# Performance work log

Measured on AMD Instinct MI355X. Metric: run time of the kernel, lower is better.

The kernel has to match this reference:

```python
import jax, jax.numpy as jnp
import numpy as np
from jax import lax

EPS = 1e-5

def _ln(x, w, b):
    m = jnp.mean(x, axis=-1, keepdims=True)
    v = jnp.mean((x - m) ** 2, axis=-1, keepdims=True)
    return (x - m) / jnp.sqrt(v + EPS) * w + b

def setup_inputs() -> dict:
    key = jax.random.key(0)
    ks = jax.random.split(key, 16)
    B, H, W, C = 4, 128, 128, 96
    N = H * W
    hidden = 192          # int(2.0 * dim)
    qk = 48               # dim // 2
    x = jax.random.normal(ks[0], (B, N, C), dtype=jnp.float32)
    # LayerNorm params
    norm_w = jnp.ones((C,), jnp.float32); norm_b = jnp.zeros((C,), jnp.float32)
    n1_w = jnp.ones((C,), jnp.float32); n1_b = jnp.zeros((C,), jnp.float32)
    n2_w = jnp.ones((C,), jnp.float32); n2_b = jnp.zeros((C,), jnp.float32)
    # Linear weights stored as [in, out]
    Wh = jax.random.normal(ks[1], (C, hidden), jnp.float32) * 0.02
    bh = jnp.zeros((hidden,), jnp.float32)
    Wqk = jax.random.normal(ks[2], (C, qk), jnp.float32) * 0.02
    bqk = jnp.zeros((qk,), jnp.float32)
    proj_w = jax.random.normal(ks[3], (C, C), jnp.float32) * 0.02
    proj_b = jnp.zeros((C,), jnp.float32)
    # per-branch affine on qk (init: normal std 0.02 / zeros, as in torch code)
    g1 = jax.random.normal(ks[4], (2, qk), jnp.float32) * 0.02
    be1 = jnp.zeros((2, qk), jnp.float32)
    g2 = jax.random.normal(ks[5], (2, qk), jnp.float32) * 0.02
    be2 = jnp.zeros((2, qk), jnp.float32)
    # SR convs (OIHW), kaiming-like init fan_out = k*k*C
    sr1_w = jax.random.normal(ks[6], (C, C, 8, 8), jnp.float32) * np.sqrt(2.0 / (8 * 8 * C))
    sr1_b = jnp.zeros((C,), jnp.float32)
    sr2_w = jax.random.normal(ks[7], (C, C, 4, 4), jnp.float32) * np.sqrt(2.0 / (4 * 4 * C))
    sr2_b = jnp.zeros((C,), jnp.float32)
    return dict(x=x, H=H, W=W, norm_w=norm_w, norm_b=norm_b, Wh=Wh, bh=bh,
                Wqk=Wqk, bqk=bqk, g1=g1, be1=be1, g2=g2, be2=be2,
                sr1_w=sr1_w, sr1_b=sr1_b, sr2_w=sr2_w, sr2_b=sr2_b,
                n1_w=n1_w, n1_b=n1_b, n2_w=n2_w, n2_b=n2_b,
                proj_w=proj_w, proj_b=proj_b)

def _sr_branch(xmap, cw, cb, lw, lb, stride):
    # xmap: [B,C,H,W]; strided conv with kernel==stride, then LN+GELU over tokens
    y = lax.conv_general_dilated(xmap, cw, (stride, stride), 'VALID',
                                 dimension_numbers=('NCHW', 'OIHW', 'NCHW'))
    y = y + cb[:, None, None]
    B, C = y.shape[0], y.shape[1]
    y = y.reshape(B, C, -1).transpose(0, 2, 1)  # [B, N', C]
    return jax.nn.gelu(_ln(y, lw, lb), approximate=False)

def reference(x, H, W, norm_w, norm_b, Wh, bh, Wqk, bqk, g1, be1, g2, be2,
              sr1_w, sr1_b, sr2_w, sr2_b, n1_w, n1_b, n2_w, n2_b, proj_w, proj_b):
    B, N, C = x.shape
    half = C // 2  # C // num_heads with num_heads=2
    nx = _ln(x, norm_w, norm_b)
    h = jax.nn.silu(nx @ Wh + bh)              # [B,N,2C]
    v, gate = h[..., :C], h[..., C:]
    xmap = nx.transpose(0, 2, 1).reshape(B, C, H, W)
    x1 = _sr_branch(xmap, sr1_w, sr1_b, n1_w, n1_b, 8)   # [B, N/64, C]
    x2 = _sr_branch(xmap, sr2_w, sr2_b, n2_w, n2_b, 4)   # [B, N/16, C]
    Z1 = jax.nn.silu(x1 @ Wqk + bqk)           # [B,N1,qk]
    QK1 = Z1[..., None, :] * g1 + be1          # [B,N1,2,qk]
    q1, k1 = QK1[..., 0, :], QK1[..., 1, :]
    Z2 = jax.nn.silu(x2 @ Wqk + bqk)
    QK2 = Z2[..., None, :] * g2 + be2
    q2, k2 = QK2[..., 0, :], QK2[..., 1, :]
    inv_n = 1.0 / N
    a1 = jnp.einsum('bnd,bmd->bnm', v[..., :half], q1) * inv_n
    A1 = jnp.square(jax.nn.relu(a1))
    V1 = jnp.einsum('bnm,bmd->bnd', A1, k1)
    a2 = jnp.einsum('bnd,bmd->bnm', v[..., half:], q2) * inv_n
    A2 = jnp.square(jax.nn.relu(a2))
    V2 = jnp.einsum('bnm,bmd->bnd', A2, k2)
    xc = jnp.concatenate([V1, V2], axis=-1)    # [B,N,C]
    value = xc * gate
    out = value @ proj_w + proj_b
    return out + xc
```

## Files before the change

### kernel.cpp

```cpp
#include <hip/hip_runtime.h>
#include <math.h>

#define NB   4
#define IH   128
#define IW   128
#define NTOK 16384
#define CC   96
#define HID  192
#define QKD  48
#define EPSF 1e-5f
#define INV_N (1.0f/16384.0f)

typedef __attribute__((ext_vector_type(8))) short sh8;
typedef __attribute__((ext_vector_type(4))) short ush4;
typedef __attribute__((ext_vector_type(4))) float f32x4;

__device__ __forceinline__ float wave_sum64(float v){
    #pragma unroll
    for (int off = 32; off > 0; off >>= 1) v += __shfl_xor(v, off, 64);
    return v;
}
__device__ __forceinline__ float siluf(float x){ return x / (1.0f + __expf(-x)); }
__device__ __forceinline__ float geluf(float x){ return 0.5f*x*(1.0f + erff(x*0.7071067811865475f)); }

__device__ __forceinline__ unsigned short f2bf(float f){
    union { float f; unsigned u; } x; x.f = f;
    unsigned u = x.u + 0x7FFFu + ((x.u >> 16) & 1u);
    return (unsigned short)(u >> 16);
}
__device__ __forceinline__ float b2f(unsigned hi16){
    union { unsigned u; float f; } c; c.u = hi16; return c.f;
}
__device__ __forceinline__ unsigned cvtpk(float a, float b){
    unsigned r;
    asm("v_cvt_pk_bf16_f32 %0, %1, %2" : "=v"(r) : "v"(a), "v"(b));
    return r;
}
__device__ __forceinline__ void swap32(unsigned &x, unsigned &y){
    asm volatile("v_permlane32_swap_b32 %0, %1" : "+v"(x), "+v"(y));
}
__device__ __forceinline__ void swap16(unsigned &x, unsigned &y){
    asm volatile("v_permlane16_swap_b32 %0, %1" : "+v"(x), "+v"(y));
}

__global__ __launch_bounds__(256) void k_ln(const float* __restrict__ x,
                                            const float* __restrict__ w,
                                            const float* __restrict__ bb,
                                            unsigned short* __restrict__ nxbf,
                                            unsigned short* __restrict__ nxim,
                                            const float* __restrict__ s1, unsigned short* __restrict__ d1, int n1,
                                            const float* __restrict__ s2, unsigned short* __restrict__ d2, int n2){
    int bid = blockIdx.x;
    if (bid >= 16384){
        int i4 = ((bid - 16384)*256 + threadIdx.x)*4;
        if (i4 < n1){
            float4 v = *(const float4*)(s1 + i4);
            unsigned u0 = cvtpk(v.x, v.y), u1 = cvtpk(v.z, v.w);
            ush4 o = {(short)u0, (short)(u0>>16), (short)u1, (short)(u1>>16)};
            *(ush4*)(d1 + i4) = o;
        } else {
            int j = i4 - n1;
            if (j < n2){
                float4 v = *(const float4*)(s2 + j);
                unsigned u0 = cvtpk(v.x, v.y), u1 = cvtpk(v.z, v.w);
                ush4 o = {(short)u0, (short)(u0>>16), (short)u1, (short)(u1>>16)};
                *(ush4*)(d2 + j) = o;
            }
        }
        return;
    }
    __shared__ unsigned short tile[4][96];
    int r = threadIdx.x >> 6;
    int row = bid*4 + r;
    int l = threadIdx.x & 63;
    const float* xr = x + (size_t)row*CC;
    float a = xr[l];
    float b = (l < 32) ? xr[64+l] : 0.0f;
    float s = wave_sum64(a + b);
    float m = s * (1.0f/96.0f);
    float d1f = a - m;
    float d2f = b - m;
    float sq = d1f*d1f + ((l < 32) ? d2f*d2f : 0.0f);
    float var = wave_sum64(sq) * (1.0f/96.0f);
    float rstd = rsqrtf(var + EPSF);
    unsigned short b1 = f2bf(d1f*rstd*w[l] + bb[l]);
    nxbf[(size_t)row*CC + l] = b1;
    tile[r][l] = b1;
    if (l < 32){
        unsigned short b2 = f2bf(d2f*rstd*w[64+l] + bb[64+l]);
        nxbf[(size_t)row*CC + 64 + l] = b2;
        tile[r][64+l] = b2;
    }
    __syncthreads();
    int t = threadIdx.x;
    if (t < 96){
        int row0 = bid*4;
        int bb2 = row0 >> 14, hw = row0 & 16383;
        ush4 v = {(short)tile[0][t], (short)tile[1][t], (short)tile[2][t], (short)tile[3][t]};
        *(ush4*)(nxim + (((size_t)(bb2*96 + t)) << 14) + hw) = v;
    }
}

__device__ __forceinline__ void conv_body(const unsigned short* __restrict__ nxim,
                                          const unsigned short* __restrict__ wbf,
                                          float* __restrict__ part,
                                          int posLog, int pdimLog, int pszLog,
                                          int kTotal, int rb, int split,
                                          unsigned short* pt, unsigned short* wt){
    const int NCH = 6;
    int tid = threadIdx.x;
    int lane = tid & 63, wid = tid >> 6, lo = lane & 15, g = lane >> 4;
    int psz = 1 << pszLog, pdim = 1 << pdimLog;
    int ksLog = 2*pszLog;
    int kb0 = split * 384;
    int cinc = (64 >> ksLog) << 14;

    int j   = tid & 15;
    int coff = (j*4) >> ksLog;
    int s   = (j*4) & (psz*psz - 1);
    int sy  = s >> pszLog, sx = s & (psz-1);
    int pAddr[4], pOff[4];
    #pragma unroll
    for (int i = 0; i < 4; i++){
        int p = (tid >> 4) + 16*i;
        int R = rb*64 + p;
        int b = R >> posLog, pp = R & ((1 << posLog) - 1);
        int pi = pp >> pdimLog, pj = pp & (pdim-1);
        pAddr[i] = (((b*96 + coff) + (kb0 >> ksLog)) << 14) + (pi*psz + sy)*IW + pj*psz + sx;
        pOff[i]  = p*72 + j*4;
    }
    int jj = tid & 7;
    int wAddr[3], wOff[3];
    #pragma unroll
    for (int i = 0; i < 3; i++){
        int o = (tid >> 3) + 32*i;
        wAddr[i] = o*kTotal + kb0 + jj*8;
        wOff[i]  = o*72 + jj*8;
    }

    f32x4 acc[6];
    #pragma unroll
    for (int ct = 0; ct < 6; ct++) acc[ct] = (f32x4){0.f,0.f,0.f,0.f};

    ush4 pr[4]; sh8 wr[3];
    #pragma unroll
    for (int i = 0; i < 4; i++) pr[i] = *(const ush4*)(nxim + pAddr[i]);
    #pragma unroll
    for (int i = 0; i < 3; i++) wr[i] = *(const sh8*)(wbf + wAddr[i]);

    for (int ch = 0; ch < NCH; ch++){
        __syncthreads();
        #pragma unroll
        for (int i = 0; i < 4; i++) *(ush4*)&pt[pOff[i]] = pr[i];
        #pragma unroll
        for (int i = 0; i < 3; i++) *(sh8*)&wt[wOff[i]] = wr[i];
        if (ch < NCH-1){
            #pragma unroll
            for (int i = 0; i < 4; i++){ pAddr[i] += cinc; pr[i] = *(const ush4*)(nxim + pAddr[i]); }
            #pragma unroll
            for (int i = 0; i < 3; i++){ wAddr[i] += 64;  wr[i] = *(const sh8*)(wbf + wAddr[i]); }
        }
        __syncthreads();

        sh8 a0 = *(const sh8*)&pt[(wid*16 + lo)*72 + g*8];
        sh8 a1 = *(const sh8*)&pt[(wid*16 + lo)*72 + 32 + g*8];
        #pragma unroll
        for (int ct = 0; ct < 6; ct++){
            sh8 b0 = *(const sh8*)&wt[(ct*16 + lo)*72 + g*8];
            sh8 b1 = *(const sh8*)&wt[(ct*16 + lo)*72 + 32 + g*8];
            acc[ct] = __builtin_amdgcn_mfma_f32_16x16x32_bf16(a0, b0, acc[ct], 0, 0, 0);
            acc[ct] = __builtin_amdgcn_mfma_f32_16x16x32_bf16(a1, b1, acc[ct], 0, 0, 0);
        }
    }

    int rowsTotal = NB << posLog;
    #pragma unroll
    for (int ct = 0; ct < 6; ct++){
        int o = ct*16 + lo;
        #pragma unroll
        for (int jx = 0; jx < 4; jx++){
            int R = rb*64 + wid*16 + g*4 + jx;
            part[((size_t)split*rowsTotal + R)*96 + o] = acc[ct][jx];
        }
    }
}

__global__ __launch_bounds__(256) void k_mid(const unsigned short* __restrict__ nxbf,
                                             const unsigned short* __restrict__ nxim,
                                             const float* __restrict__ Wh,
                                             const float* __restrict__ bh,
                                             const unsigned short* __restrict__ w1bf,
                                             const unsigned short* __restrict__ w2bf,
                                             unsigned short* __restrict__ vbuf,
                                             unsigned short* __restrict__ gate,
                                             float* __restrict__ part1,
                                             float* __restrict__ part2){
    __shared__ unsigned short smem[192*100];
    int bid = blockIdx.x;
    if (bid < 512){
        unsigned short* pt = smem;
        unsigned short* wt = smem + 64*72;
        if (bid < 256) conv_body(nxim, w1bf, part1, 8, 4, 3, 6144, bid & 15, bid >> 4, pt, wt);
        else { int b2 = bid - 256; conv_body(nxim, w2bf, part2, 10, 5, 2, 1536, b2 & 63, b2 >> 6, pt, wt); }
        return;
    }
    unsigned short* whbf = smem;
    int tid  = threadIdx.x;
    int lane = tid & 63;
    int wid  = tid >> 6;
    int lo   = lane & 15;
    int g    = lane >> 4;
    int row0 = (bid - 512)*64 + wid*16;

    #pragma unroll
    for (int it = 0; it < 36; it++){
        int pidx = tid + it*256;
        int k = pidx / 96, cp = (pidx - k*96)*2;
        float2 v = *(const float2*)&Wh[k*HID + cp];
        unsigned u = cvtpk(v.x, v.y);
        whbf[cp*100 + k]     = (unsigned short)u;
        whbf[(cp+1)*100 + k] = (unsigned short)(u >> 16);
    }

    sh8 a[3];
    {
        const unsigned short* ar = nxbf + (size_t)(row0 + lo)*CC;
        #pragma unroll
        for (int kc = 0; kc < 3; kc++)
            a[kc] = *(const sh8*)(ar + kc*32 + g*8);
    }
    __syncthreads();

    f32x4 acc[12];
    #pragma unroll
    for (int ct = 0; ct < 12; ct++) acc[ct] = (f32x4){0.f,0.f,0.f,0.f};
    #pragma unroll
    for (int ct = 0; ct < 12; ct++){
        #pragma unroll
        for (int kc = 0; kc < 3; kc++){
            sh8 bw = *(const sh8*)&whbf[(ct*16 + lo)*100 + kc*32 + g*8];
            acc[ct] = __builtin_amdgcn_mfma_f32_16x16x32_bf16(a[kc], bw, acc[ct], 0, 0, 0);
        }
    }

    #pragma unroll
    for (int ct = 0; ct < 12; ct++){
        int col = ct*16 + lo;
        float bcol = bh[col];
        #pragma unroll
        for (int j = 0; j < 4; j++){
            size_t row = row0 + g*4 + j;
            float hv = siluf(acc[ct][j] + bcol);
            unsigned short hb = (unsigned short)cvtpk(hv, hv);
            if (col < 96) vbuf[row*CC + col] = hb;
            else          gate[row*CC + col - 96] = hb;
        }
    }
}

__global__ __launch_bounds__(64) void k_reduce(const float* __restrict__ part1,
                                               const float* __restrict__ part2,
                                               const float* __restrict__ cb1, const float* __restrict__ cb2,
                                               const float* __restrict__ lw1, const float* __restrict__ lw2,
                                               const float* __restrict__ lb1, const float* __restrict__ lb2,
                                               const float* __restrict__ wqk,
                                               const float* __restrict__ bqk,
                                               const float* __restrict__ g1, const float* __restrict__ g2,
                                               const float* __restrict__ be1, const float* __restrict__ be2,
                                               unsigned short* __restrict__ qp1, unsigned short* __restrict__ qp2,
                                               unsigned short* __restrict__ kt1, unsigned short* __restrict__ kt2){
    __shared__ float xsh[96];
    int bid = blockIdx.x;
    bool fst = bid < 1024;
    int row   = fst ? bid : bid - 1024;
    int nsplit= fst ? 16 : 4;
    int rows  = fst ? 1024 : 4096;
    int Mper  = fst ? 256 : 1024;
    const float* part = fst ? part1 : part2;
    const float* cbias= fst ? cb1 : cb2;
    const float* lw   = fst ? lw1 : lw2;
    const float* lb   = fst ? lb1 : lb2;
    const float* g    = fst ? g1 : g2;
    const float* be   = fst ? be1 : be2;
    unsigned short* qp = fst ? qp1 : qp2;
    unsigned short* ktp= fst ? kt1 : kt2;

    int l = threadIdx.x;
    float y1 = 0.0f, y2 = 0.0f;
    for (int s = 0; s < nsplit; s++){
        const float* pr = part + ((size_t)s*rows + row)*96;
        y1 += pr[l];
        if (l < 32) y2 += pr[64+l];
    }
    y1 += cbias[l];
    if (l < 32) y2 += cbias[64+l];
    float s = wave_sum64(y1 + ((l < 32) ? y2 : 0.0f));
    float m = s * (1.0f/96.0f);
    float d1 = y1 - m, d2 = y2 - m;
    float var = wave_sum64(d1*d1 + ((l < 32) ? d2*d2 : 0.0f)) * (1.0f/96.0f);
    float rstd = rsqrtf(var + EPSF);
    xsh[l] = geluf(d1*rstd*lw[l] + lb[l]);
    if (l < 32) xsh[64+l] = geluf(d2*rstd*lw[64+l] + lb[64+l]);
    __syncthreads();
    if (l < 48){
        float z = bqk[l];
        #pragma unroll 4
        for (int c = 0; c < 96; c++) z += xsh[c]*wqk[c*48 + l];
        z = siluf(z);
        float qv = (z*g[l]    + be[l]) * INV_N;
        float kv =  z*g[48+l] + be[48+l];
        int b = row / Mper, p = row - b*Mper;
        qp[(size_t)row*64 + l] = f2bf(qv);
        ktp[((size_t)b*48 + l)*Mper + p] = f2bf(kv);
    } else {
        qp[(size_t)row*64 + l] = 0;
    }
}

__global__ __launch_bounds__(256) void k_attn(const unsigned short* __restrict__ vbuf,
                                              const unsigned short* __restrict__ qp1,
                                              const unsigned short* __restrict__ ktp1,
                                              const unsigned short* __restrict__ qp2,
                                              const unsigned short* __restrict__ ktp2,
                                              unsigned short* __restrict__ V1,
                                              unsigned short* __restrict__ V2){
    __shared__ unsigned short qs[2][64*72];
    __shared__ unsigned short ks[2][48*72];

    int bx   = blockIdx.x;
    int kind = (bx < 512) ? 1 : 0;
    int blk  = (bx < 512) ? bx : bx - 512;
    int tid  = threadIdx.x;
    int wid  = tid >> 6;
    int lane = tid & 63;
    int lo   = lane & 15;
    int g    = lane >> 4;
    int row0 = blk*128 + wid*32;
    int b    = row0 >> 14;

    int   M    = kind ? 1024 : 256;
    const unsigned short* qp = (kind ? qp2 : qp1) + (size_t)b*M*64;
    const unsigned short* kt = (kind ? ktp2 : ktp1) + (size_t)b*48*M;
    int   voff = kind ? 48 : 0;
    unsigned short* vout = kind ? V2 : V1;

    sh8 vb[2][2];
    #pragma unroll
    for (int nt = 0; nt < 2; nt++){
        const unsigned short* vrow = vbuf + (size_t)(row0 + nt*16 + lo)*CC + voff;
        vb[nt][0] = *(const sh8*)(vrow + g*8);
        if (g < 2) vb[nt][1] = *(const sh8*)(vrow + 32 + g*8);
        else { sh8 z = {0,0,0,0,0,0,0,0}; vb[nt][1] = z; }
    }

    int qm_ = tid >> 3, qc_ = tid & 7;
    int kd_ = tid >> 3, km_ = tid & 7;
    bool k2 = tid < 128;

    f32x4 acc[2][3];
    #pragma unroll
    for (int nt = 0; nt < 2; nt++)
        #pragma unroll
        for (int dt = 0; dt < 3; dt++) acc[nt][dt] = (f32x4){0.f,0.f,0.f,0.f};

    int nchunk = M >> 6;
    sh8 qr0 = *(const sh8*)(qp + (size_t)qm_*64 + qc_*8);
    sh8 qr1 = *(const sh8*)(qp + (size_t)(32 + qm_)*64 + qc_*8);
    sh8 kr0 = *(const sh8*)(kt + (size_t)kd_*M + km_*8);
    sh8 kr1;
    if (k2) kr1 = *(const sh8*)(kt + (size_t)(32 + kd_)*M + km_*8);

    for (int ch = 0; ch < nchunk; ch++){
        int bs = ch & 1;
        unsigned short* qb = qs[bs];
        unsigned short* kb = ks[bs];
        *(sh8*)&qb[qm_*72 + qc_*8] = qr0;
        *(sh8*)&qb[(32 + qm_)*72 + qc_*8] = qr1;
        *(sh8*)&kb[kd_*72 + km_*8] = kr0;
        if (k2) *(sh8*)&kb[(32 + kd_)*72 + km_*8] = kr1;
        __syncthreads();
        if (ch + 1 < nchunk){
            int mb2 = (ch + 1)*64;
            qr0 = *(const sh8*)(qp + (size_t)(mb2 + qm_)*64 + qc_*8);
            qr1 = *(const sh8*)(qp + (size_t)(mb2 + 32 + qm_)*64 + qc_*8);
            kr0 = *(const sh8*)(kt + (size_t)kd_*M + mb2 + km_*8);
            if (k2) kr1 = *(const sh8*)(kt + (size_t)(32 + kd_)*M + mb2 + km_*8);
        }

        f32x4 c[4][2];
        #pragma unroll
        for (int mt = 0; mt < 4; mt++){
            sh8 aq0 = *(const sh8*)&qb[(mt*16 + lo)*72 + g*8];
            sh8 aq1 = *(const sh8*)&qb[(mt*16 + lo)*72 + 32 + g*8];
            #pragma unroll
            for (int nt = 0; nt < 2; nt++){
                f32x4 cc = (f32x4){0.f,0.f,0.f,0.f};
                cc = __builtin_amdgcn_mfma_f32_16x16x32_bf16(aq0, vb[nt][0], cc, 0,0,0);
                cc = __builtin_amdgcn_mfma_f32_16x16x32_bf16(aq1, vb[nt][1], cc, 0,0,0);
                c[mt][nt] = cc;
            }
        }

        sh8 pa0[2], pa1[2];
        #pragma unroll
        for (int nt = 0; nt < 2; nt++){
            #pragma unroll
            for (int h = 0; h < 2; h++){
                f32x4 cm0 = c[h*2][nt];
                f32x4 cm1 = c[h*2+1][nt];
                float p00 = fmaxf(cm0[0], 0.f); p00 *= p00;
                float p01 = fmaxf(cm0[1], 0.f); p01 *= p01;
                float p02 = fmaxf(cm0[2], 0.f); p02 *= p02;
                float p03 = fmaxf(cm0[3], 0.f); p03 *= p03;
                float p10 = fmaxf(cm1[0], 0.f); p10 *= p10;
                float p11 = fmaxf(cm1[1], 0.f); p11 *= p11;
                float p12 = fmaxf(cm1[2], 0.f); p12 *= p12;
                float p13 = fmaxf(cm1[3], 0.f); p13 *= p13;
                unsigned a0 = cvtpk(p00, p01);
                unsigned a1 = cvtpk(p02, p03);
                unsigned b0 = cvtpk(p10, p11);
                unsigned b1 = cvtpk(p12, p13);
                swap32(a0, b0); swap16(a0, b0);
                swap32(a1, b1); swap16(a1, b1);
                union { unsigned u[4]; sh8 v; } pk;
                pk.u[0] = a0; pk.u[1] = a1; pk.u[2] = b0; pk.u[3] = b1;
                if (h == 0) pa0[nt] = pk.v; else pa1[nt] = pk.v;
            }
        }

        #pragma unroll
        for (int dt = 0; dt < 3; dt++){
            sh8 bk0 = *(const sh8*)&kb[(dt*16 + lo)*72 + g*8];
            sh8 bk1 = *(const sh8*)&kb[(dt*16 + lo)*72 + 32 + g*8];
            #pragma unroll
            for (int nt = 0; nt < 2; nt++){
                acc[nt][dt] = __builtin_amdgcn_mfma_f32_16x16x32_bf16(pa0[nt], bk0, acc[nt][dt], 0, 0, 0);
                acc[nt][dt] = __builtin_amdgcn_mfma_f32_16x16x32_bf16(pa1[nt], bk1, acc[nt][dt], 0, 0, 0);
            }
        }
    }

    #pragma unroll
    for (int nt = 0; nt < 2; nt++)
        #pragma unroll
        for (int dt = 0; dt < 3; dt++)
            #pragma unroll
            for (int j = 0; j < 4; j++)
                vout[(size_t)(row0 + nt*16 + g*4 + j)*48 + dt*16 + lo] =
                    (unsigned short)cvtpk(acc[nt][dt][j], acc[nt][dt][j]);
}

__global__ __launch_bounds__(256) void k_final(const unsigned short* __restrict__ V1,
                                               const unsigned short* __restrict__ V2,
                                               const unsigned short* __restrict__ gate,
                                               const float* __restrict__ projw,
                                               const float* __restrict__ projb,
                                               float* __restrict__ out){
    __shared__ unsigned short pjbf[96*100];
    int tid  = threadIdx.x;
    int lane = tid & 63;
    int wid  = tid >> 6;
    int lo   = lane & 15;
    int g    = lane >> 4;
    int row0 = blockIdx.x*64 + wid*16;

    #pragma unroll
    for (int it = 0; it < 18; it++){
        int pidx = tid + it*256;
        int k = pidx / 48, cp = (pidx - k*48)*2;
        float2 v = *(const float2*)&projw[k*CC + cp];
        unsigned u = cvtpk(v.x, v.y);
        pjbf[cp*100 + k]     = (unsigned short)u;
        pjbf[(cp+1)*100 + k] = (unsigned short)(u >> 16);
    }

    sh8 a[3];
    {
        size_t row = row0 + lo;
        const unsigned short* gr = gate + row*CC;
        #pragma unroll
        for (int kc = 0; kc < 3; kc++){
            int d0 = kc*32 + g*8;
            const unsigned short* xsrc = (d0 < 48) ? (V1 + row*48 + d0) : (V2 + row*48 + d0 - 48);
            union { sh8 v; unsigned u[4]; } xu, gu, pk;
            xu.v = *(const sh8*)xsrc;
            gu.v = *(const sh8*)(gr + d0);
            #pragma unroll
            for (int i = 0; i < 4; i++){
                float xl = b2f(xu.u[i] << 16),        xh = b2f(xu.u[i] & 0xffff0000u);
                float gl = b2f(gu.u[i] << 16),        gh = b2f(gu.u[i] & 0xffff0000u);
                pk.u[i] = cvtpk(xl*gl, xh*gh);
            }
            a[kc] = pk.v;
        }
    }
    __syncthreads();

    f32x4 acc[6];
    #pragma unroll
    for (int ct = 0; ct < 6; ct++) acc[ct] = (f32x4){0.f,0.f,0.f,0.f};
    #pragma unroll
    for (int ct = 0; ct < 6; ct++){
        #pragma unroll
        for (int kc = 0; kc < 3; kc++){
            sh8 bw = *(const sh8*)&pjbf[(ct*16 + lo)*100 + kc*32 + g*8];
            acc[ct] = __builtin_amdgcn_mfma_f32_16x16x32_bf16(a[kc], bw, acc[ct], 0, 0, 0);
        }
    }

    #pragma unroll
    for (int ct = 0; ct < 6; ct++){
        int col = ct*16 + lo;
        float bcol = projb[col];
        const unsigned short* xsrc = (ct < 3) ? (V1 + col) : (V2 + col - 48);
        #pragma unroll
        for (int j = 0; j < 4; j++){
            size_t row = row0 + g*4 + j;
            float xc = b2f((unsigned)xsrc[row*48] << 16);
            out[row*CC + col] = acc[ct][j] + bcol + xc;
        }
    }
}

extern "C" void kernel_launch(void* const* d_in, const int* in_sizes, int n_in,
                              void* d_out, int out_size, void* d_ws, size_t ws_size,
                              hipStream_t stream){
    const float* x      = (const float*)d_in[0];
    const float* norm_w = (const float*)d_in[3];
    const float* norm_b = (const float*)d_in[4];
    const float* Wh     = (const float*)d_in[5];
    const float* bh     = (const float*)d_in[6];
    const float* Wqk    = (const float*)d_in[7];
    const float* bqk    = (const float*)d_in[8];
    const float* g1     = (const float*)d_in[9];
    const float* be1    = (const float*)d_in[10];
    const float* g2     = (const float*)d_in[11];
    const float* be2    = (const float*)d_in[12];
    const float* sr1_w  = (const float*)d_in[13];
    const float* sr1_b  = (const float*)d_in[14];
    const float* sr2_w  = (const float*)d_in[15];
    const float* sr2_b  = (const float*)d_in[16];
    const float* n1_w   = (const float*)d_in[17];
    const float* n1_b   = (const float*)d_in[18];
    const float* n2_w   = (const float*)d_in[19];
    const float* n2_b   = (const float*)d_in[20];
    const float* proj_w = (const float*)d_in[21];
    const float* proj_b = (const float*)d_in[22];
    float* out = (float*)d_out;

    float* ws = (float*)d_ws;
    size_t off = 0;
    unsigned short* nxbf = (unsigned short*)(ws + off); off += (size_t)NB*NTOK*CC/2;
    unsigned short* nxim = (unsigned short*)(ws + off); off += (size_t)NB*NTOK*CC/2;
    unsigned short* w1bf = (unsigned short*)(ws + off); off += (size_t)96*6144/2;
    unsigned short* w2bf = (unsigned short*)(ws + off); off += (size_t)96*1536/2;
    unsigned short* vbuf = (unsigned short*)(ws + off); off += (size_t)NB*NTOK*CC/2;
    unsigned short* gate = (unsigned short*)(ws + off); off += (size_t)NB*NTOK*CC/2;
    unsigned short* qp1 = (unsigned short*)(ws + off); off += (size_t)NB*256*64/2;
    unsigned short* kt1 = (unsigned short*)(ws + off); off += (size_t)NB*48*256/2;
    unsigned short* qp2 = (unsigned short*)(ws + off); off += (size_t)NB*1024*64/2;
    unsigned short* kt2 = (unsigned short*)(ws + off); off += (size_t)NB*48*1024/2;
    float* part1= ws + off; off += (size_t)16*NB*256*96;
    float* part2= ws + off; off += (size_t)4*NB*1024*96;
    unsigned short* V1 = (unsigned short*)(ws + off); off += (size_t)NB*NTOK*48/2;
    unsigned short* V2 = (unsigned short*)(ws + off); off += (size_t)NB*NTOK*48/2;
    if (ws_size < off*sizeof(float)) return;

    k_ln   <<<17104, 256, 0, stream>>>(x, norm_w, norm_b, nxbf, nxim,
                                       sr1_w, w1bf, 96*6144, sr2_w, w2bf, 96*1536);
    k_mid  <<<1536, 256, 0, stream>>>(nxbf, nxim, Wh, bh, w1bf, w2bf, vbuf, gate, part1, part2);
    k_reduce<<<5120, 64, 0, stream>>>(part1, part2, sr1_b, sr2_b, n1_w, n2_w, n1_b, n2_b,
                                      Wqk, bqk, g1, g2, be1, be2, qp1, qp2, kt1, kt2);
    k_attn <<<1024, 256, 0, stream>>>(vbuf, qp1, kt1, qp2, kt2, V1, V2);
    k_final<<<1024, 256, 0, stream>>>(V1, V2, gate, proj_w, proj_b, out);
}
```

Before: 121.6 us.

## Fuse attention and output projection into one kernel, keeping V1/V2 in LDS

The attention kernel now handles both SR branches for each 128-row block in sequence. It stages the V1/V2 results in shared memory and then performs the gate multiply, projection, bias and residual add directly, which removes the separate k_final launch and the global round trip of V1/V2. The cost is that the grid drops from 1024 to 512 blocks, so each block does the serial work of both branches plus the projection, which reduces parallelism. LDS use per block also rises because the Q/K double buffers and the projection weights are aliased in a union.

```diff
diff --git a/kernel.cpp b/kernel.cpp
--- a/kernel.cpp
+++ b/kernel.cpp
@@ -318,151 +318,153 @@
 }
 
 __global__ __launch_bounds__(256) void k_attn(const unsigned short* __restrict__ vbuf,
+                                              const unsigned short* __restrict__ gate,
                                               const unsigned short* __restrict__ qp1,
                                               const unsigned short* __restrict__ ktp1,
                                               const unsigned short* __restrict__ qp2,
                                               const unsigned short* __restrict__ ktp2,
-                                              unsigned short* __restrict__ V1,
-                                              unsigned short* __restrict__ V2){
-    __shared__ unsigned short qs[2][64*72];
-    __shared__ unsigned short ks[2][48*72];
-
-    int bx   = blockIdx.x;
-    int kind = (bx < 512) ? 1 : 0;
-    int blk  = (bx < 512) ? bx : bx - 512;
+                                              const float* __restrict__ projw,
+                                              const float* __restrict__ projb,
+                                              float* __restrict__ out){
+    __shared__ unsigned short vt1s[4][32*56];
+    __shared__ unsigned short uni[16896];
+
+    int blk  = blockIdx.x;
     int tid  = threadIdx.x;
     int wid  = tid >> 6;
     int lane = tid & 63;
     int lo   = lane & 15;
     int g    = lane >> 4;
     int row0 = blk*128 + wid*32;
-    int b    = row0 >> 14;
-
-    int   M    = kind ? 1024 : 256;
-    const unsigned short* qp = (kind ? qp2 : qp1) + (size_t)b*M*64;
-    const unsigned short* kt = (kind ? ktp2 : ktp1) + (size_t)b*48*M;
-    int   voff = kind ? 48 : 0;
-    unsigned short* vout = kind ? V2 : V1;
-
-    sh8 vb[2][2];
-    #pragma unroll
-    for (int nt = 0; nt < 2; nt++){
-        const unsigned short* vrow = vbuf + (size_t)(row0 + nt*16 + lo)*CC + voff;
-        vb[nt][0] = *(const sh8*)(vrow + g*8);
-        if (g < 2) vb[nt][1] = *(const sh8*)(vrow + 32 + g*8);
-        else { sh8 z = {0,0,0,0,0,0,0,0}; vb[nt][1] = z; }
-    }
+    int bb   = (blk*128) >> 14;
+
+    unsigned short* vt1 = &vt1s[wid][0];
+    unsigned short* vt2 = uni + wid*1792;
+    unsigned short* pjbf = uni + 7168;
 
     int qm_ = tid >> 3, qc_ = tid & 7;
     int kd_ = tid >> 3, km_ = tid & 7;
     bool k2 = tid < 128;
 
-    f32x4 acc[2][3];
-    #pragma unroll
-    for (int nt = 0; nt < 2; nt++)
-        #pragma unroll
-        for (int dt = 0; dt < 3; dt++) acc[nt][dt] = (f32x4){0.f,0.f,0.f,0.f};
-
-    int nchunk = M >> 6;
-    sh8 qr0 = *(const sh8*)(qp + (size_t)qm_*64 + qc_*8);
-    sh8 qr1 = *(const sh8*)(qp + (size_t)(32 + qm_)*64 + qc_*8);
-    sh8 kr0 = *(const sh8*)(kt + (size_t)kd_*M + km_*8);
-    sh8 kr1;
-    if (k2) kr1 = *(const sh8*)(kt + (size_t)(32 + kd_)*M + km_*8);
-
-    for (int ch = 0; ch < nchunk; ch++){
-        int bs = ch & 1;
-        unsigned short* qb = qs[bs];
-        unsigned short* kb = ks[bs];
-        *(sh8*)&qb[qm_*72 + qc_*8] = qr0;
-        *(sh8*)&qb[(32 + qm_)*72 + qc_*8] = qr1;
-        *(sh8*)&kb[kd_*72 + km_*8] = kr0;
-        if (k2) *(sh8*)&kb[(32 + kd_)*72 + km_*8] = kr1;
-        __syncthreads();
-        if (ch + 1 < nchunk){
-            int mb2 = (ch + 1)*64;
-            qr0 = *(const sh8*)(qp + (size_t)(mb2 + qm_)*64 + qc_*8);
-            qr1 = *(const sh8*)(qp + (size_t)(mb2 + 32 + qm_)*64 + qc_*8);
-            kr0 = *(const sh8*)(kt + (size_t)kd_*M + mb2 + km_*8);
-            if (k2) kr1 = *(const sh8*)(kt + (size_t)(32 + kd_)*M + mb2 + km_*8);
-        }
-
-        f32x4 c[4][2];
-        #pragma unroll
-        for (int mt = 0; mt < 4; mt++){
-            sh8 aq0 = *(const sh8*)&qb[(mt*16 + lo)*72 + g*8];
-            sh8 aq1 = *(const sh8*)&qb[(mt*16 + lo)*72 + 32 + g*8];
+    for (int kind = 0; kind < 2; kind++){
+        int M = kind ? 1024 : 256;
+        const unsigned short* qp = (kind ? qp2 : qp1) + (size_t)bb*M*64;
+        const unsigned short* kt = (kind ? ktp2 : ktp1) + (size_t)bb*48*M;
+        int voff = kind ? 48 : 0;
+
+        sh8 vb[2][2];
+        #pragma unroll
+        for (int nt = 0; nt < 2; nt++){
+            const unsigned short* vrow = vbuf + (size_t)(row0 + nt*16 + lo)*CC + voff;
+            vb[nt][0] = *(const sh8*)(vrow + g*8);
+            if (g < 2) vb[nt][1] = *(const sh8*)(vrow + 32 + g*8);
+            else { sh8 z = {0,0,0,0,0,0,0,0}; vb[nt][1] = z; }
+        }
+
+        f32x4 acc[2][3];
+        #pragma unroll
+        for (int nt = 0; nt < 2; nt++)
+            #pragma unroll
+            for (int dt = 0; dt < 3; dt++) acc[nt][dt] = (f32x4){0.f,0.f,0.f,0.f};
+
+        int nchunk = M >> 6;
+        sh8 qr0 = *(const sh8*)(qp + (size_t)qm_*64 + qc_*8);
+        sh8 qr1 = *(const sh8*)(qp + (size_t)(32 + qm_)*64 + qc_*8);
+        sh8 kr0 = *(const sh8*)(kt + (size_t)kd_*M + km_*8);
+        sh8 kr1;
+        if (k2) kr1 = *(const sh8*)(kt + (size_t)(32 + kd_)*M + km_*8);
+
+        for (int ch = 0; ch < nchunk; ch++){
+            int bs = ch & 1;
+            unsigned short* qb = uni + bs*4608;
+            unsigned short* kb = uni + 9216 + bs*3456;
+            *(sh8*)&qb[qm_*72 + qc_*8] = qr0;
+            *(sh8*)&qb[(32 + qm_)*72 + qc_*8] = qr1;
+            *(sh8*)&kb[kd_*72 + km_*8] = kr0;
+            if (k2) *(sh8*)&kb[(32 + kd_)*72 + km_*8] = kr1;
+            __syncthreads();
+            if (ch + 1 < nchunk){
+                int mb2 = (ch + 1)*64;
+                qr0 = *(const sh8*)(qp + (size_t)(mb2 + qm_)*64 + qc_*8);
+                qr1 = *(const sh8*)(qp + (size_t)(mb2 + 32 + qm_)*64 + qc_*8);
+                kr0 = *(const sh8*)(kt + (size_t)kd_*M + mb2 + km_*8);
+                if (k2) kr1 = *(const sh8*)(kt + (size_t)(32 + kd_)*M + mb2 + km_*8);
+            }
+
+            f32x4 c[4][2];
+            #pragma unroll
+            for (int mt = 0; mt < 4; mt++){
+                sh8 aq0 = *(const sh8*)&qb[(mt*16 + lo)*72 + g*8];
+                sh8 aq1 = *(const sh8*)&qb[(mt*16 + lo)*72 + 32 + g*8];
+                #pragma unroll
+                for (int nt = 0; nt < 2; nt++){
+                    f32x4 cc = (f32x4){0.f,0.f,0.f,0.f};
+                    cc = __builtin_amdgcn_mfma_f32_16x16x32_bf16(aq0, vb[nt][0], cc, 0,0,0);
+                    cc = __builtin_amdgcn_mfma_f32_16x16x32_bf16(aq1, vb[nt][1], cc, 0,0,0);
+                    c[mt][nt] = cc;
+                }
+            }
+
+            sh8 pa0[2], pa1[2];
             #pragma unroll
             for (int nt = 0; nt < 2; nt++){
-                f32x4 cc = (f32x4){0.f,0.f,0.f,0.f};
-                cc = __builtin_amdgcn_mfma_f32_16x16x32_bf16(aq0, vb[nt][0], cc, 0,0,0);
-                cc = __builtin_amdgcn_mfma_f32_16x16x32_bf16(aq1, vb[nt][1], cc, 0,0,0);
-                c[mt][nt] = cc;
-            }
-        }
-
-        sh8 pa0[2], pa1[2];
-        #pragma unroll
-        for (int nt = 0; nt < 2; nt++){
-            #pragma unroll
-            for (int h = 0; h < 2; h++){
-                f32x4 cm0 = c[h*2][nt];
-                f32x4 cm1 = c[h*2+1][nt];
-                float p00 = fmaxf(cm0[0], 0.f); p00 *= p00;
-                float p01 = fmaxf(cm0[1], 0.f); p01 *= p01;
-                float p02 = fmaxf(cm0[2], 0.f); p02 *= p02;
-                float p03 = fmaxf(cm0[3], 0.f); p03 *= p03;
-                float p10 = fmaxf(cm1[0], 0.f); p10 *= p10;
-                float p11 = fmaxf(cm1[1], 0.f); p11 *= p11;
-                float p12 = fmaxf(cm1[2], 0.f); p12 *= p12;
-                float p13 = fmaxf(cm1[3], 0.f); p13 *= p13;
-                unsigned a0 = cvtpk(p00, p01);
-                unsigned a1 = cvtpk(p02, p03);
-                unsigned b0 = cvtpk(p10, p11);
-                unsigned b1 = cvtpk(p12, p13);
-                swap32(a0, b0); swap16(a0, b0);
-                swap32(a1, b1); swap16(a1, b1);
-                union { unsigned u[4]; sh8 v; } pk;
-                pk.u[0] = a0; pk.u[1] = a1; pk.u[2] = b0; pk.u[3] = b1;
-                if (h == 0) pa0[nt] = pk.v; else pa1[nt] = pk.v;
-            }
-        }
-
-        #pragma unroll
-        for (int dt = 0; dt < 3; dt++){
-            sh8 bk0 = *(const sh8*)&kb[(dt*16 + lo)*72 + g*8];
-            sh8 bk1 = *(const sh8*)&kb[(dt*16 + lo)*72 + 32 + g*8];
-            #pragma unroll
-            for (int nt = 0; nt < 2; nt++){
-                acc[nt][dt] = __builtin_amdgcn_mfma_f32_16x16x32_bf16(pa0[nt], bk0, acc[nt][dt], 0, 0, 0);
-                acc[nt][dt] = __builtin_amdgcn_mfma_f32_16x16x32_bf16(pa1[nt], bk1, acc[nt][dt], 0, 0, 0);
-            }
-        }
-    }
-
-    #pragma unroll
-    for (int nt = 0; nt < 2; nt++)
-        #pragma unroll
-        for (int dt = 0; dt < 3; dt++)
-            #pragma unroll
-            for (int j = 0; j < 4; j++)
-                vout[(size_t)(row0 + nt*16 + g*4 + j)*48 + dt*16 + lo] =
-                    (unsigned short)cvtpk(acc[nt][dt][j], acc[nt][dt][j]);
-}
-
-__global__ __launch_bounds__(256) void k_final(const unsigned short* __restrict__ V1,
-                                               const unsigned short* __restrict__ V2,
-                                               const unsigned short* __restrict__ gate,
-                                               const float* __restrict__ projw,
-                                               const float* __restrict__ projb,
-                                               float* __restrict__ out){
-    __shared__ unsigned short pjbf[96*100];
-    int tid  = threadIdx.x;
-    int lane = tid & 63;
-    int wid  = tid >> 6;
-    int lo   = lane & 15;
-    int g    = lane >> 4;
-    int row0 = blockIdx.x*64 + wid*16;
+                #pragma unroll
+                for (int h = 0; h < 2; h++){
+                    f32x4 cm0 = c[h*2][nt];
+                    f32x4 cm1 = c[h*2+1][nt];
+                    float p00 = fmaxf(cm0[0], 0.f); p00 *= p00;
+                    float p01 = fmaxf(cm0[1], 0.f); p01 *= p01;
+                    float p02 = fmaxf(cm0[2], 0.f); p02 *= p02;
+                    float p03 = fmaxf(cm0[3], 0.f); p03 *= p03;
+                    float p10 = fmaxf(cm1[0], 0.f); p10 *= p10;
+                    float p11 = fmaxf(cm1[1], 0.f); p11 *= p11;
+                    float p12 = fmaxf(cm1[2], 0.f); p12 *= p12;
+                    float p13 = fmaxf(cm1[3], 0.f); p13 *= p13;
+                    unsigned a0 = cvtpk(p00, p01);
+                    unsigned a1 = cvtpk(p02, p03);
+                    unsigned b0 = cvtpk(p10, p11);
+                    unsigned b1 = cvtpk(p12, p13);
+                    swap32(a0, b0); swap16(a0, b0);
+                    swap32(a1, b1); swap16(a1, b1);
+                    union { unsigned u[4]; sh8 v; } pk;
+                    pk.u[0] = a0; pk.u[1] = a1; pk.u[2] = b0; pk.u[3] = b1;
+                    if (h == 0) pa0[nt] = pk.v; else pa1[nt] = pk.v;
+                }
+            }
+
+            #pragma unroll
+            for (int dt = 0; dt < 3; dt++){
+                sh8 bk0 = *(const sh8*)&kb[(dt*16 + lo)*72 + g*8];
+                sh8 bk1 = *(const sh8*)&kb[(dt*16 + lo)*72 + 32 + g*8];
+                #pragma unroll
+                for (int nt = 0; nt < 2; nt++){
+                    acc[nt][dt] = __builtin_amdgcn_mfma_f32_16x16x32_bf16(pa0[nt], bk0, acc[nt][dt], 0, 0, 0);
+                    acc[nt][dt] = __builtin_amdgcn_mfma_f32_16x16x32_bf16(pa1[nt], bk1, acc[nt][dt], 0, 0, 0);
+                }
+            }
+        }
+
+        if (kind == 0){
+            #pragma unroll
+            for (int nt = 0; nt < 2; nt++)
+                #pragma unroll
+                for (int dt = 0; dt < 3; dt++)
+                    #pragma unroll
+                    for (int j = 0; j < 4; j++)
+                        vt1[(nt*16 + g*4 + j)*56 + dt*16 + lo] =
+                            (unsigned short)cvtpk(acc[nt][dt][j], acc[nt][dt][j]);
+        } else {
+            __syncthreads();
+            #pragma unroll
+            for (int nt = 0; nt < 2; nt++)
+                #pragma unroll
+                for (int dt = 0; dt < 3; dt++)
+                    #pragma unroll
+                    for (int j = 0; j < 4; j++)
+                        vt2[(nt*16 + g*4 + j)*56 + dt*16 + lo] =
+                            (unsigned short)cvtpk(acc[nt][dt][j], acc[nt][dt][j]);
+        }
+    }
 
     #pragma unroll
     for (int it = 0; it < 18; it++){
@@ -473,51 +475,51 @@
         pjbf[cp*100 + k]     = (unsigned short)u;
         pjbf[(cp+1)*100 + k] = (unsigned short)(u >> 16);
     }
-
-    sh8 a[3];
-    {
-        size_t row = row0 + lo;
-        const unsigned short* gr = gate + row*CC;
+    __syncthreads();
+
+    #pragma unroll
+    for (int ntp = 0; ntp < 2; ntp++){
+        int rl = ntp*16 + lo;
+        size_t grow = row0 + rl;
+        sh8 a[3];
         #pragma unroll
         for (int kc = 0; kc < 3; kc++){
             int d0 = kc*32 + g*8;
-            const unsigned short* xsrc = (d0 < 48) ? (V1 + row*48 + d0) : (V2 + row*48 + d0 - 48);
+            const unsigned short* xsrc = (d0 < 48) ? &vt1[rl*56 + d0] : &vt2[rl*56 + d0 - 48];
             union { sh8 v; unsigned u[4]; } xu, gu, pk;
             xu.v = *(const sh8*)xsrc;
-            gu.v = *(const sh8*)(gr + d0);
+            gu.v = *(const sh8*)(gate + grow*CC + d0);
             #pragma unroll
             for (int i = 0; i < 4; i++){
-                float xl = b2f(xu.u[i] << 16),        xh = b2f(xu.u[i] & 0xffff0000u);
-                float gl = b2f(gu.u[i] << 16),        gh = b2f(gu.u[i] & 0xffff0000u);
+                float xl = b2f(xu.u[i] << 16), xh = b2f(xu.u[i] & 0xffff0000u);
+                float gl = b2f(gu.u[i] << 16), gh = b2f(gu.u[i] & 0xffff0000u);
                 pk.u[i] = cvtpk(xl*gl, xh*gh);
             }
             a[kc] = pk.v;
         }
-    }
-    __syncthreads();
-
-    f32x4 acc[6];
-    #pragma unroll
-    for (int ct = 0; ct < 6; ct++) acc[ct] = (f32x4){0.f,0.f,0.f,0.f};
-    #pragma unroll
-    for (int ct = 0; ct < 6; ct++){
-        #pragma unroll
-        for (int kc = 0; kc < 3; kc++){
-            sh8 bw = *(const sh8*)&pjbf[(ct*16 + lo)*100 + kc*32 + g*8];
-            acc[ct] = __builtin_amdgcn_mfma_f32_16x16x32_bf16(a[kc], bw, acc[ct], 0, 0, 0);
-        }
-    }
-
-    #pragma unroll
-    for (int ct = 0; ct < 6; ct++){
-        int col = ct*16 + lo;
-        float bcol = projb[col];
-        const unsigned short* xsrc = (ct < 3) ? (V1 + col) : (V2 + col - 48);
-        #pragma unroll
-        for (int j = 0; j < 4; j++){
-            size_t row = row0 + g*4 + j;
-            float xc = b2f((unsigned)xsrc[row*48] << 16);
-            out[row*CC + col] = acc[ct][j] + bcol + xc;
+
+        f32x4 pacc[6];
+        #pragma unroll
+        for (int ct = 0; ct < 6; ct++) pacc[ct] = (f32x4){0.f,0.f,0.f,0.f};
+        #pragma unroll
+        for (int ct = 0; ct < 6; ct++){
+            #pragma unroll
+            for (int kc = 0; kc < 3; kc++){
+                sh8 bw = *(const sh8*)&pjbf[(ct*16 + lo)*100 + kc*32 + g*8];
+                pacc[ct] = __builtin_amdgcn_mfma_f32_16x16x32_bf16(a[kc], bw, pacc[ct], 0, 0, 0);
+            }
+        }
+
+        #pragma unroll
+        for (int ct = 0; ct < 6; ct++){
+            int col = ct*16 + lo;
+            float bcol = projb[col];
+            #pragma unroll
+            for (int j = 0; j < 4; j++){
+                int rl2 = ntp*16 + g*4 + j;
+                unsigned short xb = (col < 48) ? vt1[rl2*56 + col] : vt2[rl2*56 + col - 48];
+                out[(size_t)(row0 + rl2)*CC + col] = pacc[ct][j] + bcol + b2f((unsigned)xb << 16);
+            }
         }
     }
 }
@@ -562,8 +564,6 @@
     unsigned short* kt2 = (unsigned short*)(ws + off); off += (size_t)NB*48*1024/2;
     float* part1= ws + off; off += (size_t)16*NB*256*96;
     float* part2= ws + off; off += (size_t)4*NB*1024*96;
-    unsigned short* V1 = (unsigned short*)(ws + off); off += (size_t)NB*NTOK*48/2;
-    unsigned short* V2 = (unsigned short*)(ws + off); off += (size_t)NB*NTOK*48/2;
     if (ws_size < off*sizeof(float)) return;
 
     k_ln   <<<17104, 256, 0, stream>>>(x, norm_w, norm_b, nxbf, nxim,
@@ -571,6 +571,5 @@
     k_mid  <<<1536, 256, 0, stream>>>(nxbf, nxim, Wh, bh, w1bf, w2bf, vbuf, gate, part1, part2);
     k_reduce<<<5120, 64, 0, stream>>>(part1, part2, sr1_b, sr2_b, n1_w, n2_w, n1_b, n2_b,
                                       Wqk, bqk, g1, g2, be1, be2, qp1, qp2, kt1, kt2);
-    k_attn <<<1024, 256, 0, stream>>>(vbuf, qp1, kt1, qp2, kt2, V1, V2);
-    k_final<<<1024, 256, 0, stream>>>(V1, V2, gate, proj_w, proj_b, out);
-}
+    k_attn <<<512, 256, 0, stream>>>(vbuf, gate, qp1, kt1, qp2, kt2, proj_w, proj_b, out);
+}
```

After: 116.9 us. -3.9%, faster.
